# Kernel tuning notes

Measured on AMD Instinct MI355X. Metric: run time of the kernel, lower is better.

## Reference

```python
import jax, jax.numpy as jnp
import numpy as np

MAX_ITER = 20
TAU = 1.0

def setup_inputs() -> dict:
    key = jax.random.key(0)
    s = jax.random.normal(key, (256, 512, 512), dtype=jnp.float32)
    return {"s": s}

def reference(s):
    # Sinkhorn-Knopp in log space. With nrows=ncols=None and square input,
    # the per-batch loop in the original reduces to full-matrix normalization.
    # Even iterations normalize along the last axis (dim=1 of each 2D matrix),
    # odd iterations along the row axis.
    log_s = s / TAU
    for i in range(MAX_ITER):
        axis = 2 if i % 2 == 0 else 1
        log_s = log_s - jax.nn.logsumexp(log_s, axis=axis, keepdims=True)
    return jnp.exp(log_s)
```

## Files before the change

### kernel.cpp

```cpp
#include <hip/hip_runtime.h>

#define N 512
#define WAVES 16
#define BLOCK (WAVES * 64)
#define ROWS_PER_WAVE (N / WAVES)

__global__ __launch_bounds__(BLOCK, 1)
void sinkhorn_kernel(const float* __restrict__ A, float* __restrict__ Out) {
    __shared__ float swv[N];
    __shared__ float sinvS[N];
    __shared__ float spart[WAVES][N];

    const float* __restrict__ Ab = A   + (size_t)blockIdx.x * N * N;
    float* __restrict__ Eb       = Out + (size_t)blockIdx.x * N * N;
    const int tid  = threadIdx.x;
    const int lane = tid & 63;
    const int wave = tid >> 6;

    {
        float t0=0.f,t1=0.f,t2=0.f,t3=0.f,t4=0.f,t5=0.f,t6=0.f,t7=0.f;
        #pragma unroll 4
        for (int k = 0; k < ROWS_PER_WAVE; ++k) {
            const int row = k * WAVES + wave;
            const float4* R = (const float4*)(Ab + (size_t)row * N);
            float4*       W = (float4*)(Eb + (size_t)row * N);
            const float4 x0 = R[lane];
            const float4 x1 = R[lane + 64];

            const float e0 = __expf(x0.x), e1 = __expf(x0.y),
                        e2 = __expf(x0.z), e3 = __expf(x0.w);
            const float e4 = __expf(x1.x), e5 = __expf(x1.y),
                        e6 = __expf(x1.z), e7 = __expf(x1.w);

            W[lane]      = make_float4(e0, e1, e2, e3);
            W[lane + 64] = make_float4(e4, e5, e6, e7);

            float S = ((e0 + e1) + (e2 + e3)) + ((e4 + e5) + (e6 + e7));
            #pragma unroll
            for (int m = 1; m < 64; m <<= 1) S += __shfl_xor(S, m, 64);

            const float inv = 1.0f / S;
            if (lane == 0) sinvS[row] = inv;

            t0 += e0 * inv; t1 += e1 * inv; t2 += e2 * inv; t3 += e3 * inv;
            t4 += e4 * inv; t5 += e5 * inv; t6 += e6 * inv; t7 += e7 * inv;
        }
        ((float4*)spart[wave])[lane]      = make_float4(t0, t1, t2, t3);
        ((float4*)spart[wave])[lane + 64] = make_float4(t4, t5, t6, t7);
        __syncthreads();
        if (tid < N) {
            float s = 0.f;
            #pragma unroll
            for (int w = 0; w < WAVES; ++w) s += spart[w][tid];
            swv[tid] = 1.0f / s;
        }
        __syncthreads();
    }

    for (int pass = 1; pass < 10; ++pass) {
        const float4 w0 = ((const float4*)swv)[lane];
        const float4 w1 = ((const float4*)swv)[lane + 64];
        float t0=0.f,t1=0.f,t2=0.f,t3=0.f,t4=0.f,t5=0.f,t6=0.f,t7=0.f;

        #pragma unroll 4
        for (int k = 0; k < ROWS_PER_WAVE; ++k) {
            const int row = k * WAVES + wave;
            const float4* R = (const float4*)(Eb + (size_t)row * N);
            const float4 a0 = R[lane];
            const float4 a1 = R[lane + 64];

            const float s01 = a0.x * w0.x + a0.y * w0.y;
            const float s23 = a0.z * w0.z + a0.w * w0.w;
            const float s45 = a1.x * w1.x + a1.y * w1.y;
            const float s67 = a1.z * w1.z + a1.w * w1.w;
            float S = (s01 + s23) + (s45 + s67);
            #pragma unroll
            for (int m = 1; m < 64; m <<= 1) S += __shfl_xor(S, m, 64);

            const float inv = 1.0f / S;
            if (lane == 0) sinvS[row] = inv;

            t0 += a0.x * inv; t1 += a0.y * inv; t2 += a0.z * inv; t3 += a0.w * inv;
            t4 += a1.x * inv; t5 += a1.y * inv; t6 += a1.z * inv; t7 += a1.w * inv;
        }

        ((float4*)spart[wave])[lane]      = make_float4(t0, t1, t2, t3);
        ((float4*)spart[wave])[lane + 64] = make_float4(t4, t5, t6, t7);
        __syncthreads();
        if (tid < N) {
            float s = 0.f;
            #pragma unroll
            for (int w = 0; w < WAVES; ++w) s += spart[w][tid];
            swv[tid] = 1.0f / s;
        }
        __syncthreads();
    }

    {
        const float4 w0 = ((const float4*)swv)[lane];
        const float4 w1 = ((const float4*)swv)[lane + 64];
        #pragma unroll 4
        for (int k = 0; k < ROWS_PER_WAVE; ++k) {
            const int row = k * WAVES + wave;
            float4* W = (float4*)(Eb + (size_t)row * N);
            const float4 a0 = W[lane];
            const float4 a1 = W[lane + 64];
            const float c = sinvS[row];

            float4 o0, o1;
            o0.x = a0.x * (c * w0.x);
            o0.y = a0.y * (c * w0.y);
            o0.z = a0.z * (c * w0.z);
            o0.w = a0.w * (c * w0.w);
            o1.x = a1.x * (c * w1.x);
            o1.y = a1.y * (c * w1.y);
            o1.z = a1.z * (c * w1.z);
            o1.w = a1.w * (c * w1.w);

            W[lane]      = o0;
            W[lane + 64] = o1;
        }
    }
}

extern "C" void kernel_launch(void* const* d_in, const int* in_sizes, int n_in,
                              void* d_out, int out_size, void* d_ws, size_t ws_size,
                              hipStream_t stream) {
    const float* s = (const float*)d_in[0];
    float* out = (float*)d_out;
    const int nmat = in_sizes[0] / (N * N);
    sinkhorn_kernel<<<nmat, BLOCK, 0, stream>>>(s, out);
}
```

Before: 825.5 us.

## Store intermediate exp matrix as fp16 and recompute exp from input at final pass

Stores the exponentiated matrix as packed fp16 in the first half of the output buffer instead of fp32. The nine scaling-vector passes then read half as many bytes, and the working set is more likely to stay in on-chip cache. The final pass recomputes exp from the fp32 input rather than reading the stored copy, so the output keeps full precision in that step. The trade-off is that the row and column scaling factors are now computed from fp16-rounded values, which adds some numerical error to the result.

```diff
diff --git a/kernel.cpp b/kernel.cpp
--- a/kernel.cpp
+++ b/kernel.cpp
@@ -1,4 +1,5 @@
 #include <hip/hip_runtime.h>
+#include <hip/hip_fp16.h>
 
 #define N 512
 #define WAVES 16
@@ -11,8 +12,10 @@
     __shared__ float sinvS[N];
     __shared__ float spart[WAVES][N];
 
-    const float* __restrict__ Ab = A   + (size_t)blockIdx.x * N * N;
-    float* __restrict__ Eb       = Out + (size_t)blockIdx.x * N * N;
+    const float* __restrict__ Ab = A   + (size_t)blockIdx.x * (N * N);
+    float* __restrict__ Ob       = Out + (size_t)blockIdx.x * (N * N);
+    __half* __restrict__ Eh      = (__half*)Ob;
+
     const int tid  = threadIdx.x;
     const int lane = tid & 63;
     const int wave = tid >> 6;
@@ -23,17 +26,20 @@
         for (int k = 0; k < ROWS_PER_WAVE; ++k) {
             const int row = k * WAVES + wave;
             const float4* R = (const float4*)(Ab + (size_t)row * N);
-            float4*       W = (float4*)(Eb + (size_t)row * N);
-            const float4 x0 = R[lane];
-            const float4 x1 = R[lane + 64];
+            const float4 x0 = R[2 * lane];
+            const float4 x1 = R[2 * lane + 1];
 
             const float e0 = __expf(x0.x), e1 = __expf(x0.y),
                         e2 = __expf(x0.z), e3 = __expf(x0.w);
             const float e4 = __expf(x1.x), e5 = __expf(x1.y),
                         e6 = __expf(x1.z), e7 = __expf(x1.w);
 
-            W[lane]      = make_float4(e0, e1, e2, e3);
-            W[lane + 64] = make_float4(e4, e5, e6, e7);
+            float4 pk;
+            ((__half2*)&pk)[0] = __floats2half2_rn(e0, e1);
+            ((__half2*)&pk)[1] = __floats2half2_rn(e2, e3);
+            ((__half2*)&pk)[2] = __floats2half2_rn(e4, e5);
+            ((__half2*)&pk)[3] = __floats2half2_rn(e6, e7);
+            ((float4*)(Eh + (size_t)row * N))[lane] = pk;
 
             float S = ((e0 + e1) + (e2 + e3)) + ((e4 + e5) + (e6 + e7));
             #pragma unroll
@@ -45,8 +51,8 @@
             t0 += e0 * inv; t1 += e1 * inv; t2 += e2 * inv; t3 += e3 * inv;
             t4 += e4 * inv; t5 += e5 * inv; t6 += e6 * inv; t7 += e7 * inv;
         }
-        ((float4*)spart[wave])[lane]      = make_float4(t0, t1, t2, t3);
-        ((float4*)spart[wave])[lane + 64] = make_float4(t4, t5, t6, t7);
+        ((float4*)spart[wave])[2 * lane]     = make_float4(t0, t1, t2, t3);
+        ((float4*)spart[wave])[2 * lane + 1] = make_float4(t4, t5, t6, t7);
         __syncthreads();
         if (tid < N) {
             float s = 0.f;
@@ -58,21 +64,24 @@
     }
 
     for (int pass = 1; pass < 10; ++pass) {
-        const float4 w0 = ((const float4*)swv)[lane];
-        const float4 w1 = ((const float4*)swv)[lane + 64];
+        const float4 wa = ((const float4*)swv)[2 * lane];
+        const float4 wb = ((const float4*)swv)[2 * lane + 1];
         float t0=0.f,t1=0.f,t2=0.f,t3=0.f,t4=0.f,t5=0.f,t6=0.f,t7=0.f;
 
-        #pragma unroll 4
+        #pragma unroll 8
         for (int k = 0; k < ROWS_PER_WAVE; ++k) {
             const int row = k * WAVES + wave;
-            const float4* R = (const float4*)(Eb + (size_t)row * N);
-            const float4 a0 = R[lane];
-            const float4 a1 = R[lane + 64];
+            const float4 raw = ((const float4*)(Eh + (size_t)row * N))[lane];
+            const __half2* h = (const __half2*)&raw;
+            const float2 f01 = __half22float2(h[0]);
+            const float2 f23 = __half22float2(h[1]);
+            const float2 f45 = __half22float2(h[2]);
+            const float2 f67 = __half22float2(h[3]);
 
-            const float s01 = a0.x * w0.x + a0.y * w0.y;
-            const float s23 = a0.z * w0.z + a0.w * w0.w;
-            const float s45 = a1.x * w1.x + a1.y * w1.y;
-            const float s67 = a1.z * w1.z + a1.w * w1.w;
+            const float s01 = f01.x * wa.x + f01.y * wa.y;
+            const float s23 = f23.x * wa.z + f23.y * wa.w;
+            const float s45 = f45.x * wb.x + f45.y * wb.y;
+            const float s67 = f67.x * wb.z + f67.y * wb.w;
             float S = (s01 + s23) + (s45 + s67);
             #pragma unroll
             for (int m = 1; m < 64; m <<= 1) S += __shfl_xor(S, m, 64);
@@ -80,12 +89,14 @@
             const float inv = 1.0f / S;
             if (lane == 0) sinvS[row] = inv;
 
-            t0 += a0.x * inv; t1 += a0.y * inv; t2 += a0.z * inv; t3 += a0.w * inv;
-            t4 += a1.x * inv; t5 += a1.y * inv; t6 += a1.z * inv; t7 += a1.w * inv;
+            t0 += f01.x * inv; t1 += f01.y * inv;
+            t2 += f23.x * inv; t3 += f23.y * inv;
+            t4 += f45.x * inv; t5 += f45.y * inv;
+            t6 += f67.x * inv; t7 += f67.y * inv;
         }
 
-        ((float4*)spart[wave])[lane]      = make_float4(t0, t1, t2, t3);
-        ((float4*)spart[wave])[lane + 64] = make_float4(t4, t5, t6, t7);
+        ((float4*)spart[wave])[2 * lane]     = make_float4(t0, t1, t2, t3);
+        ((float4*)spart[wave])[2 * lane + 1] = make_float4(t4, t5, t6, t7);
         __syncthreads();
         if (tid < N) {
             float s = 0.f;
@@ -102,20 +113,21 @@
         #pragma unroll 4
         for (int k = 0; k < ROWS_PER_WAVE; ++k) {
             const int row = k * WAVES + wave;
-            float4* W = (float4*)(Eb + (size_t)row * N);
-            const float4 a0 = W[lane];
-            const float4 a1 = W[lane + 64];
+            const float4* R = (const float4*)(Ab + (size_t)row * N);
+            float4*       W = (float4*)(Ob + (size_t)row * N);
+            const float4 x0 = R[lane];
+            const float4 x1 = R[lane + 64];
             const float c = sinvS[row];
 
             float4 o0, o1;
-            o0.x = a0.x * (c * w0.x);
-            o0.y = a0.y * (c * w0.y);
-            o0.z = a0.z * (c * w0.z);
-            o0.w = a0.w * (c * w0.w);
-            o1.x = a1.x * (c * w1.x);
-            o1.y = a1.y * (c * w1.y);
-            o1.z = a1.z * (c * w1.z);
-            o1.w = a1.w * (c * w1.w);
+            o0.x = __expf(x0.x) * (c * w0.x);
+            o0.y = __expf(x0.y) * (c * w0.y);
+            o0.z = __expf(x0.z) * (c * w0.z);
+            o0.w = __expf(x0.w) * (c * w0.w);
+            o1.x = __expf(x1.x) * (c * w1.x);
+            o1.y = __expf(x1.y) * (c * w1.y);
+            o1.z = __expf(x1.z) * (c * w1.z);
+            o1.w = __expf(x1.w) * (c * w1.w);
 
             W[lane]      = o0;
             W[lane + 64] = o1;
```

Result: faster. 751.3 us (-9.0%).
